# Kernel tuning notes

Hardware: AMD Instinct MI355X
Metric: run time of the kernel (lower is better)

The kernel has to match this reference:

```python
import jax, jax.numpy as jnp
import numpy as np


def setup_inputs() -> dict:
    key = jax.random.key(0)
    sentence = jax.random.normal(key, (8192, 256), dtype=jnp.float32)
    return {"sentence": sentence}


def reference(sentence):
    # [N, N] unnormalized attention weights
    unnormalized = jnp.matmul(sentence, sentence.T)
    # row-sum normalization (no softmax, per original module)
    normalized = unnormalized / jnp.sum(unnormalized, axis=-1, keepdims=True)
    # [N, D] reweighted vectors
    return jnp.matmul(normalized, sentence)
```

## Files before the change

### kernel.cpp

```cpp
#include <hip/hip_runtime.h>


#define N 8192
#define D 256
#define TAU 8.0
#define NFMAX 64

#define WS_CNT_OFF    0
#define WS_FLAG_OFF   16
#define WS_M_OFF      32800
#define WS_DEN_OFF    294944
#define WS_LIST_OFF   360480
#define WS_LEAF_OFF   360608
#define WS_TPART_OFF  401408
#define WS_MPART_OFF  1048576
#define WS_XT_OFF     16777216

__global__ __launch_bounds__(256) void fusedA_k(const float* __restrict__ X,
                                                float* __restrict__ Mpart,
                                                float* __restrict__ XT,
                                                double* __restrict__ Tpart,
                                                int* __restrict__ cnt,
                                                int* __restrict__ flagslot) {
    __shared__ __align__(16) char smem[16896];
    const int tid = threadIdx.x;
    const int bx  = blockIdx.x;

    if (bx < 512) {
        float4* As4 = (float4*)smem;
        float4* Bs4 = (float4*)(smem + 8192);
        const int tx = tid & 15;
        const int ty = tid >> 4;
        const int dt = (bx & 3) * 64;
        const int kt = ((bx >> 2) & 3) * 64;
        const int z  = bx >> 4;
        const int rchunk = z * 256;

        float acc[4][4];
        #pragma unroll
        for (int a = 0; a < 4; ++a)
            #pragma unroll
            for (int b = 0; b < 4; ++b) acc[a][b] = 0.0f;

        for (int c = 0; c < 8; ++c) {
            const int rb = rchunk + c * 32;
            for (int i = tid; i < 512; i += 256) {
                const int rr = i >> 4;
                const int f4 = i & 15;
                const float4* xrow = (const float4*)(X + (size_t)(rb + rr) * D);
                As4[rr * 16 + f4] = xrow[(kt >> 2) + f4];
                Bs4[rr * 16 + f4] = xrow[(dt >> 2) + f4];
            }
            __syncthreads();
            #pragma unroll 8
            for (int r = 0; r < 32; ++r) {
                const float4 a4 = As4[r * 16 + ty];
                const float4 b4 = Bs4[r * 16 + tx];
                acc[0][0] += a4.x * b4.x; acc[0][1] += a4.x * b4.y; acc[0][2] += a4.x * b4.z; acc[0][3] += a4.x * b4.w;
                acc[1][0] += a4.y * b4.x; acc[1][1] += a4.y * b4.y; acc[1][2] += a4.y * b4.z; acc[1][3] += a4.y * b4.w;
                acc[2][0] += a4.z * b4.x; acc[2][1] += a4.z * b4.y; acc[2][2] += a4.z * b4.z; acc[2][3] += a4.z * b4.w;
                acc[3][0] += a4.w * b4.x; acc[3][1] += a4.w * b4.y; acc[3][2] += a4.w * b4.z; acc[3][3] += a4.w * b4.w;
            }
            __syncthreads();
        }

        float* Mp = Mpart + (size_t)z * 65536;
        #pragma unroll
        for (int a = 0; a < 4; ++a) {
            const int mr = kt + ty * 4 + a;
            *(float4*)(Mp + (size_t)mr * D + dt + tx * 4) =
                make_float4(acc[a][0], acc[a][1], acc[a][2], acc[a][3]);
        }
    } else if (bx < 1024) {
        float (*tile)[65] = (float(*)[65])smem;
        const int b  = bx - 512;
        const int j0 = (b & 127) * 64;
        const int k0 = (b >> 7) * 64;

        const int c4 = tid & 15;
        const int r  = tid >> 4;
        #pragma unroll
        for (int i = 0; i < 4; ++i) {
            const int row = r + i * 16;
            const float4 v = *(const float4*)(X + (size_t)(j0 + row) * D + k0 + c4 * 4);
            tile[row][c4 * 4 + 0] = v.x;
            tile[row][c4 * 4 + 1] = v.y;
            tile[row][c4 * 4 + 2] = v.z;
            tile[row][c4 * 4 + 3] = v.w;
        }
        __syncthreads();

        const int jj4 = tid & 15;
        const int kk  = tid >> 4;
        #pragma unroll
        for (int i = 0; i < 4; ++i) {
            const int k = kk + i * 16;
            float4 o;
            o.x = tile[jj4 * 4 + 0][k];
            o.y = tile[jj4 * 4 + 1][k];
            o.z = tile[jj4 * 4 + 2][k];
            o.w = tile[jj4 * 4 + 3][k];
            *(float4*)(XT + (size_t)(k0 + k) * N + j0 + jj4 * 4) = o;
        }
    } else {
        const int b  = bx - 1024;
        const int r0 = b * 64;
        double s = 0.0;
        #pragma unroll 8
        for (int r = 0; r < 64; ++r)
            s += (double)X[(size_t)(r0 + r) * D + tid];
        Tpart[b * 256 + tid] = s;

        const int gi = b * 256 + tid;
        if (gi < N) flagslot[gi] = 0;
        if (gi == 0) *cnt = 0;
    }
}

__global__ __launch_bounds__(256) void fusedB_k(const float* __restrict__ X,
                                                const float* __restrict__ Mpart,
                                                float* __restrict__ M,
                                                const double* __restrict__ Tpart,
                                                double* __restrict__ den,
                                                int* __restrict__ cnt,
                                                unsigned short* __restrict__ list,
                                                int* __restrict__ flagslot) {
    __shared__ __align__(16) char smem[36864];
    const int tid = threadIdx.x;
    const int bx  = blockIdx.x;

    if (bx < 64) {
        const int e4 = bx * 256 + tid;
        const float4* P4 = (const float4*)Mpart;
        float4 s = make_float4(0.f, 0.f, 0.f, 0.f);
        #pragma unroll 8
        for (int z = 0; z < 32; ++z) {
            const float4 p = P4[(size_t)z * 16384 + e4];
            s.x += p.x; s.y += p.y; s.z += p.z; s.w += p.w;
        }
        ((float4*)M)[e4] = s;
    } else {
        float*  xs    = (float*)smem;
        double* Ts    = (double*)(smem + 32768);
        double (*dpart)[8] = (double(*)[8])(smem + 34816);

        const int r0 = (bx - 64) * 32;
        {
            const float4* xb = (const float4*)(X + (size_t)r0 * D);
            float4* xs4 = (float4*)xs;
            #pragma unroll
            for (int i = 0; i < 8; ++i) xs4[tid + i * 256] = xb[tid + i * 256];
            double t = 0.0;
            #pragma unroll 8
            for (int b = 0; b < 128; ++b) t += Tpart[b * 256 + tid];
            Ts[tid] = t;
        }
        __syncthreads();

        {
            const int r = tid & 31;
            const int c = tid >> 5;
            double s = 0.0;
            #pragma unroll
            for (int j = 0; j < 32; ++j) {
                const int k = c * 32 + ((j + r) & 31);
                s += (double)xs[r * 256 + k] * Ts[k];
            }
            dpart[r][c] = s;
        }
        __syncthreads();

        if (tid < 32) {
            double s = 0.0;
            #pragma unroll
            for (int c = 0; c < 8; ++c) s += dpart[tid][c];
            const int i = r0 + tid;
            den[i] = s;
            if (fabs(s) < TAU) {
                int p = atomicAdd(cnt, 1);
                if (p < NFMAX) {
                    list[p] = (unsigned short)i;
                    flagslot[i] = p + 1;
                }
            }
        }
    }
}

__global__ __launch_bounds__(256) void den_emu_k(const float* __restrict__ X,
                                                 const float* __restrict__ XT,
                                                 const int* __restrict__ cnt,
                                                 const unsigned short* __restrict__ list,
                                                 float* __restrict__ leafbuf) {
    __shared__ __align__(16) float xiT[256][8];
    __shared__ __align__(16) float sv[8][512];
    const int tid = threadIdx.x;
    int nflag = *cnt;
    if (nflag > NFMAX) nflag = NFMAX;
    const int groups = (nflag + 7) >> 3;
    const int jc  = blockIdx.x;
    const int jb2 = jc * 256 + tid;
    const float2* XT2 = (const float2*)XT;

    for (int g = blockIdx.y; g < groups; g += gridDim.y) {
        const int base = g * 8;
        #pragma unroll
        for (int q = 0; q < 8; ++q) {
            float v = 0.0f;
            if (base + q < nflag)
                v = X[(size_t)list[base + q] * D + tid];
            xiT[tid][q] = v;
        }
        __syncthreads();

        float ax[8], ay[8];
        #pragma unroll
        for (int q = 0; q < 8; ++q) { ax[q] = 0.0f; ay[q] = 0.0f; }

        #pragma unroll 4
        for (int k = 0; k < 256; ++k) {
            const float2 v  = XT2[(size_t)k * (N / 2) + jb2];
            const float4 a0 = *(const float4*)&xiT[k][0];
            const float4 a1 = *(const float4*)&xiT[k][4];
            ax[0] = fmaf(a0.x, v.x, ax[0]); ay[0] = fmaf(a0.x, v.y, ay[0]);
            ax[1] = fmaf(a0.y, v.x, ax[1]); ay[1] = fmaf(a0.y, v.y, ay[1]);
            ax[2] = fmaf(a0.z, v.x, ax[2]); ay[2] = fmaf(a0.z, v.y, ay[2]);
            ax[3] = fmaf(a0.w, v.x, ax[3]); ay[3] = fmaf(a0.w, v.y, ay[3]);
            ax[4] = fmaf(a1.x, v.x, ax[4]); ay[4] = fmaf(a1.x, v.y, ay[4]);
            ax[5] = fmaf(a1.y, v.x, ax[5]); ay[5] = fmaf(a1.y, v.y, ay[5]);
            ax[6] = fmaf(a1.z, v.x, ax[6]); ay[6] = fmaf(a1.z, v.y, ay[6]);
            ax[7] = fmaf(a1.w, v.x, ax[7]); ay[7] = fmaf(a1.w, v.y, ay[7]);
        }
        #pragma unroll
        for (int q = 0; q < 8; ++q)
            ((float2*)sv[q])[tid] = make_float2(ax[q], ay[q]);
        __syncthreads();

        if (tid < 32) {
            const int q = tid >> 2;
            const int quarter = tid & 3;
            if (base + q < nflag) {
                const float* a = &sv[q][quarter * 128];
                float r0 = a[0], r1 = a[1], r2 = a[2], r3 = a[3];
                float r4 = a[4], r5 = a[5], r6 = a[6], r7 = a[7];
                for (int i2 = 8; i2 < 128; i2 += 8) {
                    r0 += a[i2 + 0]; r1 += a[i2 + 1]; r2 += a[i2 + 2]; r3 += a[i2 + 3];
                    r4 += a[i2 + 4]; r5 += a[i2 + 5]; r6 += a[i2 + 6]; r7 += a[i2 + 7];
                }
                leafbuf[(base + q) * 64 + jc * 4 + quarter] =
                    ((r0 + r1) + (r2 + r3)) + ((r4 + r5) + (r6 + r7));
            }
        }
        __syncthreads();
    }
}

__global__ __launch_bounds__(256) void out_k(const float* __restrict__ X,
                                             const float* __restrict__ M,
                                             const double* __restrict__ den,
                                             const int* __restrict__ flagslot,
                                             const float* __restrict__ leafbuf,
                                             float* __restrict__ out) {
    __shared__ __align__(16) float xs[16 * 256];
    __shared__ float inv_den[16];

    const int tid = threadIdx.x;
    const int r0  = blockIdx.x * 16;

    {
        const float4* xb = (const float4*)(X + (size_t)r0 * D);
        float4* xs4 = (float4*)xs;
        #pragma unroll
        for (int i = 0; i < 4; ++i) xs4[tid + i * 256] = xb[tid + i * 256];
    }
    if (tid < 16) {
        const int i = r0 + tid;
        double dv = den[i];
        const int s = flagslot[i];
        if (s) {
            const float* lf = &leafbuf[(size_t)(s - 1) * 64];
            float t[64];
            #pragma unroll
            for (int l = 0; l < 64; ++l) t[l] = lf[l];
            #pragma unroll
            for (int nn = 32; nn >= 1; nn >>= 1) {
                #pragma unroll
                for (int l = 0; l < nn; ++l) t[l] = t[2 * l] + t[2 * l + 1];
            }
            dv = (double)t[0];
        }
        inv_den[tid] = (float)(1.0 / dv);
    }
    __syncthreads();

    const int d0 = (tid & 63) * 4;
    const int rg = (tid >> 6) * 4;
    float4 acc[4];
    #pragma unroll
    for (int i = 0; i < 4; ++i) acc[i] = make_float4(0.f, 0.f, 0.f, 0.f);

    #pragma unroll 4
    for (int k = 0; k < 256; ++k) {
        const float4 m4 = *(const float4*)(M + (size_t)k * D + d0);
        #pragma unroll
        for (int i = 0; i < 4; ++i) {
            const float xv = xs[(rg + i) * 256 + k];
            acc[i].x += xv * m4.x;
            acc[i].y += xv * m4.y;
            acc[i].z += xv * m4.z;
            acc[i].w += xv * m4.w;
        }
    }

    #pragma unroll
    for (int i = 0; i < 4; ++i) {
        const int r = rg + i;
        const float inv = inv_den[r];
        float4 o;
        o.x = acc[i].x * inv;
        o.y = acc[i].y * inv;
        o.z = acc[i].z * inv;
        o.w = acc[i].w * inv;
        *(float4*)(out + (size_t)(r0 + r) * D + d0) = o;
    }
}

extern "C" void kernel_launch(void* const* d_in, const int* in_sizes, int n_in,
                              void* d_out, int out_size, void* d_ws, size_t ws_size,
                              hipStream_t stream) {
    const float* X = (const float*)d_in[0];
    float* out = (float*)d_out;

    char* ws = (char*)d_ws;
    int*            cnt      = (int*)(ws + WS_CNT_OFF);
    int*            flagslot = (int*)(ws + WS_FLAG_OFF);
    float*          M        = (float*)(ws + WS_M_OFF);
    double*         den      = (double*)(ws + WS_DEN_OFF);
    unsigned short* list     = (unsigned short*)(ws + WS_LIST_OFF);
    float*          leaf     = (float*)(ws + WS_LEAF_OFF);
    double*         Tpart    = (double*)(ws + WS_TPART_OFF);
    float*          Mpart    = (float*)(ws + WS_MPART_OFF);
    float*          XT       = (float*)(ws + WS_XT_OFF);

    fusedA_k<<<dim3(1152), dim3(256), 0, stream>>>(X, Mpart, XT, Tpart, cnt, flagslot);
    fusedB_k<<<dim3(320),  dim3(256), 0, stream>>>(X, Mpart, M, Tpart, den, cnt, list, flagslot);
    den_emu_k<<<dim3(16, 8), dim3(256), 0, stream>>>(X, XT, cnt, list, leaf);
    out_k<<<dim3(512), dim3(256), 0, stream>>>(X, M, den, flagslot, leaf, out);
}
```

Before: 139.3 us.

## Fuse four kernels into one cooperative persistent kernel with grid syncs

Merges the four separate launches (partial Gram and transpose, reduce and denominators, flagged-row recomputation, output GEMM) into a single cooperative kernel of 512 blocks. Phases are separated by grid.sync(). The output GEMM's accumulation is moved ahead of the last grid barrier so it overlaps with the flagged-row work, and only the scaling waits for the leaf sums. This removes launch gaps and the kernel-boundary drains between stages. In exchange it adds grid-wide barrier cost, requires all 512 blocks to be co-resident, and leaves the earlier phases with fewer blocks than the old grids used.

```diff
diff --git a/kernel.cpp b/kernel.cpp
--- a/kernel.cpp
+++ b/kernel.cpp
@@ -1,4 +1,7 @@
 #include <hip/hip_runtime.h>
+#include <hip/hip_cooperative_groups.h>
+
+namespace cg = cooperative_groups;
 
 
 #define N 8192
@@ -16,31 +19,43 @@
 #define WS_MPART_OFF  1048576
 #define WS_XT_OFF     16777216
 
-__global__ __launch_bounds__(256) void fusedA_k(const float* __restrict__ X,
-                                                float* __restrict__ Mpart,
-                                                float* __restrict__ XT,
-                                                double* __restrict__ Tpart,
-                                                int* __restrict__ cnt,
-                                                int* __restrict__ flagslot) {
-    __shared__ __align__(16) char smem[16896];
+__global__ __launch_bounds__(256, 2) void fused_all_k(const float* __restrict__ X,
+                                                      float* __restrict__ out,
+                                                      void* __restrict__ wsv) {
+    char* ws = (char*)wsv;
+    int*            cnt      = (int*)(ws + WS_CNT_OFF);
+    int*            flagslot = (int*)(ws + WS_FLAG_OFF);
+    float*          M        = (float*)(ws + WS_M_OFF);
+    double*         den      = (double*)(ws + WS_DEN_OFF);
+    unsigned short* list     = (unsigned short*)(ws + WS_LIST_OFF);
+    float*          leafbuf  = (float*)(ws + WS_LEAF_OFF);
+    double*         Tpart    = (double*)(ws + WS_TPART_OFF);
+    float*          Mpart    = (float*)(ws + WS_MPART_OFF);
+    float*          XT       = (float*)(ws + WS_XT_OFF);
+
+    __shared__ __align__(16) char smem[36864];
     const int tid = threadIdx.x;
-    const int bx  = blockIdx.x;
-
-    if (bx < 512) {
+    const int b   = blockIdx.x;
+    cg::grid_group grid = cg::this_grid();
+
+    if (b < 32) flagslot[b * 256 + tid] = 0;
+    if (b == 0 && tid == 0) *cnt = 0;
+
+    {
         float4* As4 = (float4*)smem;
         float4* Bs4 = (float4*)(smem + 8192);
         const int tx = tid & 15;
         const int ty = tid >> 4;
-        const int dt = (bx & 3) * 64;
-        const int kt = ((bx >> 2) & 3) * 64;
-        const int z  = bx >> 4;
+        const int dt = (b & 3) * 64;
+        const int kt = ((b >> 2) & 3) * 64;
+        const int z  = b >> 4;
         const int rchunk = z * 256;
 
         float acc[4][4];
         #pragma unroll
         for (int a = 0; a < 4; ++a)
             #pragma unroll
-            for (int b = 0; b < 4; ++b) acc[a][b] = 0.0f;
+            for (int c = 0; c < 4; ++c) acc[a][c] = 0.0f;
 
         for (int c = 0; c < 8; ++c) {
             const int rb = rchunk + c * 32;
@@ -64,16 +79,18 @@
             __syncthreads();
         }
 
-        float* Mp = Mpart + (size_t)z * 65536;
+        float* Mp = Mpart + (size_t)(b >> 4) * 65536;
         #pragma unroll
         for (int a = 0; a < 4; ++a) {
             const int mr = kt + ty * 4 + a;
             *(float4*)(Mp + (size_t)mr * D + dt + tx * 4) =
                 make_float4(acc[a][0], acc[a][1], acc[a][2], acc[a][3]);
         }
-    } else if (bx < 1024) {
+    }
+    __syncthreads();
+
+    {
         float (*tile)[65] = (float(*)[65])smem;
-        const int b  = bx - 512;
         const int j0 = (b & 127) * 64;
         const int k0 = (b >> 7) * 64;
 
@@ -102,35 +119,21 @@
             o.w = tile[jj4 * 4 + 3][k];
             *(float4*)(XT + (size_t)(k0 + k) * N + j0 + jj4 * 4) = o;
         }
-    } else {
-        const int b  = bx - 1024;
-        const int r0 = b * 64;
+    }
+
+    if (b < 128) {
+        const int r0c = b * 64;
         double s = 0.0;
         #pragma unroll 8
         for (int r = 0; r < 64; ++r)
-            s += (double)X[(size_t)(r0 + r) * D + tid];
+            s += (double)X[(size_t)(r0c + r) * D + tid];
         Tpart[b * 256 + tid] = s;
-
-        const int gi = b * 256 + tid;
-        if (gi < N) flagslot[gi] = 0;
-        if (gi == 0) *cnt = 0;
-    }
-}
-
-__global__ __launch_bounds__(256) void fusedB_k(const float* __restrict__ X,
-                                                const float* __restrict__ Mpart,
-                                                float* __restrict__ M,
-                                                const double* __restrict__ Tpart,
-                                                double* __restrict__ den,
-                                                int* __restrict__ cnt,
-                                                unsigned short* __restrict__ list,
-                                                int* __restrict__ flagslot) {
-    __shared__ __align__(16) char smem[36864];
-    const int tid = threadIdx.x;
-    const int bx  = blockIdx.x;
-
-    if (bx < 64) {
-        const int e4 = bx * 256 + tid;
+    }
+
+    grid.sync();
+
+    if (b < 64) {
+        const int e4 = b * 256 + tid;
         const float4* P4 = (const float4*)Mpart;
         float4 s = make_float4(0.f, 0.f, 0.f, 0.f);
         #pragma unroll 8
@@ -139,12 +142,12 @@
             s.x += p.x; s.y += p.y; s.z += p.z; s.w += p.w;
         }
         ((float4*)M)[e4] = s;
-    } else {
+    } else if (b < 320) {
         float*  xs    = (float*)smem;
         double* Ts    = (double*)(smem + 32768);
         double (*dpart)[8] = (double(*)[8])(smem + 34816);
 
-        const int r0 = (bx - 64) * 32;
+        const int r0 = (b - 64) * 32;
         {
             const float4* xb = (const float4*)(X + (size_t)r0 * D);
             float4* xs4 = (float4*)xs;
@@ -152,7 +155,7 @@
             for (int i = 0; i < 8; ++i) xs4[tid + i * 256] = xb[tid + i * 256];
             double t = 0.0;
             #pragma unroll 8
-            for (int b = 0; b < 128; ++b) t += Tpart[b * 256 + tid];
+            for (int bb = 0; bb < 128; ++bb) t += Tpart[bb * 256 + tid];
             Ts[tid] = t;
         }
         __syncthreads();
@@ -185,111 +188,84 @@
             }
         }
     }
-}
-
-__global__ __launch_bounds__(256) void den_emu_k(const float* __restrict__ X,
-                                                 const float* __restrict__ XT,
-                                                 const int* __restrict__ cnt,
-                                                 const unsigned short* __restrict__ list,
-                                                 float* __restrict__ leafbuf) {
-    __shared__ __align__(16) float xiT[256][8];
-    __shared__ __align__(16) float sv[8][512];
-    const int tid = threadIdx.x;
+
+    grid.sync();
+
     int nflag = *cnt;
     if (nflag > NFMAX) nflag = NFMAX;
     const int groups = (nflag + 7) >> 3;
-    const int jc  = blockIdx.x;
-    const int jb2 = jc * 256 + tid;
-    const float2* XT2 = (const float2*)XT;
-
-    for (int g = blockIdx.y; g < groups; g += gridDim.y) {
-        const int base = g * 8;
-        #pragma unroll
-        for (int q = 0; q < 8; ++q) {
-            float v = 0.0f;
-            if (base + q < nflag)
-                v = X[(size_t)list[base + q] * D + tid];
-            xiT[tid][q] = v;
-        }
-        __syncthreads();
-
-        float ax[8], ay[8];
-        #pragma unroll
-        for (int q = 0; q < 8; ++q) { ax[q] = 0.0f; ay[q] = 0.0f; }
-
-        #pragma unroll 4
-        for (int k = 0; k < 256; ++k) {
-            const float2 v  = XT2[(size_t)k * (N / 2) + jb2];
-            const float4 a0 = *(const float4*)&xiT[k][0];
-            const float4 a1 = *(const float4*)&xiT[k][4];
-            ax[0] = fmaf(a0.x, v.x, ax[0]); ay[0] = fmaf(a0.x, v.y, ay[0]);
-            ax[1] = fmaf(a0.y, v.x, ax[1]); ay[1] = fmaf(a0.y, v.y, ay[1]);
-            ax[2] = fmaf(a0.z, v.x, ax[2]); ay[2] = fmaf(a0.z, v.y, ay[2]);
-            ax[3] = fmaf(a0.w, v.x, ax[3]); ay[3] = fmaf(a0.w, v.y, ay[3]);
-            ax[4] = fmaf(a1.x, v.x, ax[4]); ay[4] = fmaf(a1.x, v.y, ay[4]);
-            ax[5] = fmaf(a1.y, v.x, ax[5]); ay[5] = fmaf(a1.y, v.y, ay[5]);
-            ax[6] = fmaf(a1.z, v.x, ax[6]); ay[6] = fmaf(a1.z, v.y, ay[6]);
-            ax[7] = fmaf(a1.w, v.x, ax[7]); ay[7] = fmaf(a1.w, v.y, ay[7]);
-        }
-        #pragma unroll
-        for (int q = 0; q < 8; ++q)
-            ((float2*)sv[q])[tid] = make_float2(ax[q], ay[q]);
-        __syncthreads();
-
-        if (tid < 32) {
-            const int q = tid >> 2;
-            const int quarter = tid & 3;
-            if (base + q < nflag) {
-                const float* a = &sv[q][quarter * 128];
-                float r0 = a[0], r1 = a[1], r2 = a[2], r3 = a[3];
-                float r4 = a[4], r5 = a[5], r6 = a[6], r7 = a[7];
-                for (int i2 = 8; i2 < 128; i2 += 8) {
-                    r0 += a[i2 + 0]; r1 += a[i2 + 1]; r2 += a[i2 + 2]; r3 += a[i2 + 3];
-                    r4 += a[i2 + 4]; r5 += a[i2 + 5]; r6 += a[i2 + 6]; r7 += a[i2 + 7];
-                }
-                leafbuf[(base + q) * 64 + jc * 4 + quarter] =
-                    ((r0 + r1) + (r2 + r3)) + ((r4 + r5) + (r6 + r7));
-            }
-        }
-        __syncthreads();
-    }
-}
-
-__global__ __launch_bounds__(256) void out_k(const float* __restrict__ X,
-                                             const float* __restrict__ M,
-                                             const double* __restrict__ den,
-                                             const int* __restrict__ flagslot,
-                                             const float* __restrict__ leafbuf,
-                                             float* __restrict__ out) {
-    __shared__ __align__(16) float xs[16 * 256];
-    __shared__ float inv_den[16];
-
-    const int tid = threadIdx.x;
-    const int r0  = blockIdx.x * 16;
-
+
+    if (b < 128) {
+        const int jc = b & 15;
+        const int gq = b >> 4;
+        if (gq < groups) {
+            float* xiT  = (float*)smem;
+            float* sv   = (float*)(smem + 8192);
+            float* part = (float*)(smem + 8192 + 16384);
+
+            const int base = gq * 8;
+            #pragma unroll
+            for (int q = 0; q < 8; ++q) {
+                float v = 0.0f;
+                if (base + q < nflag)
+                    v = X[(size_t)list[base + q] * D + tid];
+                xiT[tid * 8 + q] = v;
+            }
+            __syncthreads();
+
+            const float2* XT2 = (const float2*)XT;
+            const int jb2 = jc * 256 + tid;
+            float ax[8], ay[8];
+            #pragma unroll
+            for (int q = 0; q < 8; ++q) { ax[q] = 0.0f; ay[q] = 0.0f; }
+
+            #pragma unroll 4
+            for (int k = 0; k < 256; ++k) {
+                const float2 v  = XT2[(size_t)k * (N / 2) + jb2];
+                const float4 a0 = *(const float4*)&xiT[k * 8 + 0];
+                const float4 a1 = *(const float4*)&xiT[k * 8 + 4];
+                ax[0] = fmaf(a0.x, v.x, ax[0]); ay[0] = fmaf(a0.x, v.y, ay[0]);
+                ax[1] = fmaf(a0.y, v.x, ax[1]); ay[1] = fmaf(a0.y, v.y, ay[1]);
+                ax[2] = fmaf(a0.z, v.x, ax[2]); ay[2] = fmaf(a0.z, v.y, ay[2]);
+                ax[3] = fmaf(a0.w, v.x, ax[3]); ay[3] = fmaf(a0.w, v.y, ay[3]);
+                ax[4] = fmaf(a1.x, v.x, ax[4]); ay[4] = fmaf(a1.x, v.y, ay[4]);
+                ax[5] = fmaf(a1.y, v.x, ax[5]); ay[5] = fmaf(a1.y, v.y, ay[5]);
+                ax[6] = fmaf(a1.z, v.x, ax[6]); ay[6] = fmaf(a1.z, v.y, ay[6]);
+                ax[7] = fmaf(a1.w, v.x, ax[7]); ay[7] = fmaf(a1.w, v.y, ay[7]);
+            }
+            #pragma unroll
+            for (int q = 0; q < 8; ++q)
+                ((float2*)(sv + q * 512))[tid] = make_float2(ax[q], ay[q]);
+            __syncthreads();
+
+            {
+                const int q = tid >> 5, quarter = (tid >> 3) & 3, P = tid & 7;
+                const float* a = sv + q * 512 + quarter * 128;
+                float r = a[P];
+                #pragma unroll
+                for (int i2 = 8; i2 < 128; i2 += 8) r += a[i2 + P];
+                part[tid] = r;
+            }
+            __syncthreads();
+            if (tid < 32) {
+                const int q = tid >> 2, quarter = tid & 3;
+                const float* p = part + tid * 8;
+                const float leafv = ((p[0] + p[1]) + (p[2] + p[3])) +
+                                    ((p[4] + p[5]) + (p[6] + p[7]));
+                if (base + q < nflag)
+                    leafbuf[(size_t)(base + q) * 64 + jc * 4 + quarter] = leafv;
+            }
+        }
+    }
+    __syncthreads();
+
+    const int r0o = b * 16;
+    float* xs = (float*)smem;
     {
-        const float4* xb = (const float4*)(X + (size_t)r0 * D);
+        const float4* xb = (const float4*)(X + (size_t)r0o * D);
         float4* xs4 = (float4*)xs;
         #pragma unroll
         for (int i = 0; i < 4; ++i) xs4[tid + i * 256] = xb[tid + i * 256];
-    }
-    if (tid < 16) {
-        const int i = r0 + tid;
-        double dv = den[i];
-        const int s = flagslot[i];
-        if (s) {
-            const float* lf = &leafbuf[(size_t)(s - 1) * 64];
-            float t[64];
-            #pragma unroll
-            for (int l = 0; l < 64; ++l) t[l] = lf[l];
-            #pragma unroll
-            for (int nn = 32; nn >= 1; nn >>= 1) {
-                #pragma unroll
-                for (int l = 0; l < nn; ++l) t[l] = t[2 * l] + t[2 * l + 1];
-            }
-            dv = (double)t[0];
-        }
-        inv_den[tid] = (float)(1.0 / dv);
     }
     __syncthreads();
 
@@ -311,6 +287,29 @@
             acc[i].w += xv * m4.w;
         }
     }
+
+    grid.sync();
+
+    float* inv_den = (float*)smem;
+    if (tid < 16) {
+        const int i = r0o + tid;
+        double dv = den[i];
+        const int s = flagslot[i];
+        if (s) {
+            const float* lf = &leafbuf[(size_t)(s - 1) * 64];
+            float t[64];
+            #pragma unroll
+            for (int l = 0; l < 64; ++l) t[l] = lf[l];
+            #pragma unroll
+            for (int nn = 32; nn >= 1; nn >>= 1) {
+                #pragma unroll
+                for (int l = 0; l < nn; ++l) t[l] = t[2 * l] + t[2 * l + 1];
+            }
+            dv = (double)t[0];
+        }
+        inv_den[tid] = (float)(1.0 / dv);
+    }
+    __syncthreads();
 
     #pragma unroll
     for (int i = 0; i < 4; ++i) {
@@ -321,7 +320,7 @@
         o.y = acc[i].y * inv;
         o.z = acc[i].z * inv;
         o.w = acc[i].w * inv;
-        *(float4*)(out + (size_t)(r0 + r) * D + d0) = o;
+        *(float4*)(out + (size_t)(r0o + r) * D + d0) = o;
     }
 }
 
@@ -330,20 +329,9 @@
                               hipStream_t stream) {
     const float* X = (const float*)d_in[0];
     float* out = (float*)d_out;
-
-    char* ws = (char*)d_ws;
-    int*            cnt      = (int*)(ws + WS_CNT_OFF);
-    int*            flagslot = (int*)(ws + WS_FLAG_OFF);
-    float*          M        = (float*)(ws + WS_M_OFF);
-    double*         den      = (double*)(ws + WS_DEN_OFF);
-    unsigned short* list     = (unsigned short*)(ws + WS_LIST_OFF);
-    float*          leaf     = (float*)(ws + WS_LEAF_OFF);
-    double*         Tpart    = (double*)(ws + WS_TPART_OFF);
-    float*          Mpart    = (float*)(ws + WS_MPART_OFF);
-    float*          XT       = (float*)(ws + WS_XT_OFF);
-
-    fusedA_k<<<dim3(1152), dim3(256), 0, stream>>>(X, Mpart, XT, Tpart, cnt, flagslot);
-    fusedB_k<<<dim3(320),  dim3(256), 0, stream>>>(X, Mpart, M, Tpart, den, cnt, list, flagslot);
-    den_emu_k<<<dim3(16, 8), dim3(256), 0, stream>>>(X, XT, cnt, list, leaf);
-    out_k<<<dim3(512), dim3(256), 0, stream>>>(X, M, den, flagslot, leaf, out);
+    void* wsv = d_ws;
+
+    void* args[] = { (void*)&X, (void*)&out, (void*)&wsv };
+    hipLaunchCooperativeKernel((const void*)fused_all_k, dim3(512), dim3(256),
+                               args, 0, stream);
 }
```

After: 308.9 us. 122% more time.

## Merge denominator emulation into output kernel and patch flagged rows afterward

Applied to the files above, without the earlier changes.

The separate den_emu and out kernels become one launch. Its first 128 blocks compute the emulated leaf sums for flagged rows, and the remaining blocks compute output tiles of 32 rows, twice the old 16. A small fixup kernel then rescales each flagged row by den/emu, so the output kernel no longer waits on leaf sums. This runs the two stages concurrently and halves reads of M per output row, in exchange for an extra launch and a read-modify-write on flagged rows, plus slightly different rounding from the float ratio multiply.

```diff
diff --git a/kernel.cpp b/kernel.cpp
--- a/kernel.cpp
+++ b/kernel.cpp
@@ -187,32 +187,41 @@
     }
 }
 
-__global__ __launch_bounds__(256) void den_emu_k(const float* __restrict__ X,
+__global__ __launch_bounds__(256) void emu_out_k(const float* __restrict__ X,
                                                  const float* __restrict__ XT,
+                                                 const float* __restrict__ M,
+                                                 const double* __restrict__ den,
                                                  const int* __restrict__ cnt,
                                                  const unsigned short* __restrict__ list,
-                                                 float* __restrict__ leafbuf) {
-    __shared__ __align__(16) float xiT[256][8];
-    __shared__ __align__(16) float sv[8][512];
+                                                 float* __restrict__ leafbuf,
+                                                 float* __restrict__ out) {
+    __shared__ __align__(16) char smem[33024];
     const int tid = threadIdx.x;
-    int nflag = *cnt;
-    if (nflag > NFMAX) nflag = NFMAX;
-    const int groups = (nflag + 7) >> 3;
-    const int jc  = blockIdx.x;
-    const int jb2 = jc * 256 + tid;
-    const float2* XT2 = (const float2*)XT;
-
-    for (int g = blockIdx.y; g < groups; g += gridDim.y) {
+    const int b   = blockIdx.x;
+
+    if (b < 128) {
+        int nflag = *cnt;
+        if (nflag > NFMAX) nflag = NFMAX;
+        const int groups = (nflag + 7) >> 3;
+        const int jc = b & 15;
+        const int g  = b >> 4;
+        if (g >= groups) return;
+
+        float* xiT = (float*)smem;
+        float* sv  = (float*)(smem + 8192);
+
         const int base = g * 8;
         #pragma unroll
         for (int q = 0; q < 8; ++q) {
             float v = 0.0f;
             if (base + q < nflag)
                 v = X[(size_t)list[base + q] * D + tid];
-            xiT[tid][q] = v;
-        }
-        __syncthreads();
-
+            xiT[tid * 8 + q] = v;
+        }
+        __syncthreads();
+
+        const float2* XT2 = (const float2*)XT;
+        const int jb2 = jc * 256 + tid;
         float ax[8], ay[8];
         #pragma unroll
         for (int q = 0; q < 8; ++q) { ax[q] = 0.0f; ay[q] = 0.0f; }
@@ -220,8 +229,8 @@
         #pragma unroll 4
         for (int k = 0; k < 256; ++k) {
             const float2 v  = XT2[(size_t)k * (N / 2) + jb2];
-            const float4 a0 = *(const float4*)&xiT[k][0];
-            const float4 a1 = *(const float4*)&xiT[k][4];
+            const float4 a0 = *(const float4*)&xiT[k * 8 + 0];
+            const float4 a1 = *(const float4*)&xiT[k * 8 + 4];
             ax[0] = fmaf(a0.x, v.x, ax[0]); ay[0] = fmaf(a0.x, v.y, ay[0]);
             ax[1] = fmaf(a0.y, v.x, ax[1]); ay[1] = fmaf(a0.y, v.y, ay[1]);
             ax[2] = fmaf(a0.z, v.x, ax[2]); ay[2] = fmaf(a0.z, v.y, ay[2]);
@@ -233,77 +242,50 @@
         }
         #pragma unroll
         for (int q = 0; q < 8; ++q)
-            ((float2*)sv[q])[tid] = make_float2(ax[q], ay[q]);
+            ((float2*)(sv + q * 512))[tid] = make_float2(ax[q], ay[q]);
         __syncthreads();
 
         if (tid < 32) {
-            const int q = tid >> 2;
-            const int quarter = tid & 3;
+            const int q = tid >> 2, quarter = tid & 3;
             if (base + q < nflag) {
-                const float* a = &sv[q][quarter * 128];
+                const float* a = sv + q * 512 + quarter * 128;
                 float r0 = a[0], r1 = a[1], r2 = a[2], r3 = a[3];
                 float r4 = a[4], r5 = a[5], r6 = a[6], r7 = a[7];
                 for (int i2 = 8; i2 < 128; i2 += 8) {
                     r0 += a[i2 + 0]; r1 += a[i2 + 1]; r2 += a[i2 + 2]; r3 += a[i2 + 3];
                     r4 += a[i2 + 4]; r5 += a[i2 + 5]; r6 += a[i2 + 6]; r7 += a[i2 + 7];
                 }
-                leafbuf[(base + q) * 64 + jc * 4 + quarter] =
+                leafbuf[(size_t)(base + q) * 64 + jc * 4 + quarter] =
                     ((r0 + r1) + (r2 + r3)) + ((r4 + r5) + (r6 + r7));
             }
         }
-        __syncthreads();
-    }
-}
-
-__global__ __launch_bounds__(256) void out_k(const float* __restrict__ X,
-                                             const float* __restrict__ M,
-                                             const double* __restrict__ den,
-                                             const int* __restrict__ flagslot,
-                                             const float* __restrict__ leafbuf,
-                                             float* __restrict__ out) {
-    __shared__ __align__(16) float xs[16 * 256];
-    __shared__ float inv_den[16];
-
-    const int tid = threadIdx.x;
-    const int r0  = blockIdx.x * 16;
-
+        return;
+    }
+
+    float* xs      = (float*)smem;
+    float* inv_den = (float*)(smem + 32768);
+
+    const int r0 = (b - 128) * 32;
     {
         const float4* xb = (const float4*)(X + (size_t)r0 * D);
         float4* xs4 = (float4*)xs;
         #pragma unroll
-        for (int i = 0; i < 4; ++i) xs4[tid + i * 256] = xb[tid + i * 256];
-    }
-    if (tid < 16) {
-        const int i = r0 + tid;
-        double dv = den[i];
-        const int s = flagslot[i];
-        if (s) {
-            const float* lf = &leafbuf[(size_t)(s - 1) * 64];
-            float t[64];
-            #pragma unroll
-            for (int l = 0; l < 64; ++l) t[l] = lf[l];
-            #pragma unroll
-            for (int nn = 32; nn >= 1; nn >>= 1) {
-                #pragma unroll
-                for (int l = 0; l < nn; ++l) t[l] = t[2 * l] + t[2 * l + 1];
-            }
-            dv = (double)t[0];
-        }
-        inv_den[tid] = (float)(1.0 / dv);
-    }
+        for (int i = 0; i < 8; ++i) xs4[tid + i * 256] = xb[tid + i * 256];
+    }
+    if (tid < 32) inv_den[tid] = (float)(1.0 / den[r0 + tid]);
     __syncthreads();
 
     const int d0 = (tid & 63) * 4;
-    const int rg = (tid >> 6) * 4;
-    float4 acc[4];
+    const int rg = (tid >> 6) * 8;
+    float4 acc[8];
     #pragma unroll
-    for (int i = 0; i < 4; ++i) acc[i] = make_float4(0.f, 0.f, 0.f, 0.f);
+    for (int i = 0; i < 8; ++i) acc[i] = make_float4(0.f, 0.f, 0.f, 0.f);
 
     #pragma unroll 4
     for (int k = 0; k < 256; ++k) {
         const float4 m4 = *(const float4*)(M + (size_t)k * D + d0);
         #pragma unroll
-        for (int i = 0; i < 4; ++i) {
+        for (int i = 0; i < 8; ++i) {
             const float xv = xs[(rg + i) * 256 + k];
             acc[i].x += xv * m4.x;
             acc[i].y += xv * m4.y;
@@ -313,7 +295,7 @@
     }
 
     #pragma unroll
-    for (int i = 0; i < 4; ++i) {
+    for (int i = 0; i < 8; ++i) {
         const int r = rg + i;
         const float inv = inv_den[r];
         float4 o;
@@ -323,6 +305,33 @@
         o.w = acc[i].w * inv;
         *(float4*)(out + (size_t)(r0 + r) * D + d0) = o;
     }
+}
+
+__global__ __launch_bounds__(256) void fixup_k(const int* __restrict__ cnt,
+                                               const unsigned short* __restrict__ list,
+                                               const float* __restrict__ leafbuf,
+                                               const double* __restrict__ den,
+                                               float* __restrict__ out) {
+    int nflag = *cnt;
+    if (nflag > NFMAX) nflag = NFMAX;
+    const int b = blockIdx.x;
+    if (b >= nflag) return;
+
+    const int row = list[b];
+    const float* lf = &leafbuf[(size_t)b * 64];
+    float t[64];
+    #pragma unroll
+    for (int l = 0; l < 64; ++l) t[l] = lf[l];
+    #pragma unroll
+    for (int nn = 32; nn >= 1; nn >>= 1) {
+        #pragma unroll
+        for (int l = 0; l < nn; ++l) t[l] = t[2 * l] + t[2 * l + 1];
+    }
+    const double emu = (double)t[0];
+    const float ratio = (float)(den[row] * (1.0 / emu));
+
+    const int idx = (int)row * D + threadIdx.x;
+    out[idx] = out[idx] * ratio;
 }
 
 extern "C" void kernel_launch(void* const* d_in, const int* in_sizes, int n_in,
@@ -344,6 +353,6 @@
 
     fusedA_k<<<dim3(1152), dim3(256), 0, stream>>>(X, Mpart, XT, Tpart, cnt, flagslot);
     fusedB_k<<<dim3(320),  dim3(256), 0, stream>>>(X, Mpart, M, Tpart, den, cnt, list, flagslot);
-    den_emu_k<<<dim3(16, 8), dim3(256), 0, stream>>>(X, XT, cnt, list, leaf);
-    out_k<<<dim3(512), dim3(256), 0, stream>>>(X, M, den, flagslot, leaf, out);
-}
+    emu_out_k<<<dim3(384), dim3(256), 0, stream>>>(X, XT, M, den, cnt, list, leaf, out);
+    fixup_k<<<dim3(NFMAX), dim3(256), 0, stream>>>(cnt, list, leaf, den, out);
+}
```

New measurement: 120.3 us. -13.7%, faster.
